# Optimization experiments

Hardware: AMD Instinct MI355X
Metric: run time of the kernel (lower is better)

The kernel has to match this reference:

```python
import jax, jax.numpy as jnp
import numpy as np

E = 8           # ensemble size
D_IN = 512      # input_dim (state+action)
H = 1024        # hidden size, arch=[1024, 1024]
D_OUT = 1       # output_dim (Q value)
LN_EPS = 1e-5


def setup_inputs() -> dict:
    key = jax.random.key(0)
    ks = jax.random.split(key, 8)
    s1 = 1.0 / np.sqrt(D_IN)
    s2 = 1.0 / np.sqrt(H)
    return {
        "x": jax.random.normal(ks[0], (16384, D_IN), dtype=jnp.float32),
        # stacked per-ensemble parameters: leading axis E
        "W1": jax.random.uniform(ks[1], (E, D_IN, H), jnp.float32, -s1, s1),
        "b1": jax.random.uniform(ks[2], (E, H), jnp.float32, -s1, s1),
        "g1": jnp.ones((E, H), jnp.float32),
        "be1": jnp.zeros((E, H), jnp.float32),
        "W2": jax.random.uniform(ks[3], (E, H, H), jnp.float32, -s2, s2),
        "b2": jax.random.uniform(ks[4], (E, H), jnp.float32, -s2, s2),
        "g2": jnp.ones((E, H), jnp.float32),
        "be2": jnp.zeros((E, H), jnp.float32),
        "W3": jax.random.uniform(ks[5], (E, H, D_OUT), jnp.float32, -s2, s2),
        "b3": jax.random.uniform(ks[6], (E, D_OUT), jnp.float32, -s2, s2),
    }


def _layer_norm(h, g, b):
    # h: [E, B, H]; g, b: [E, H] -> broadcast over batch
    mu = jnp.mean(h, axis=-1, keepdims=True)
    var = jnp.mean(jnp.square(h - mu), axis=-1, keepdims=True)
    return (h - mu) * jax.lax.rsqrt(var + LN_EPS) * g[:, None, :] + b[:, None, :]


def reference(x, W1, b1, g1, be1, W2, b2, g2, be2, W3, b3):
    # Layer 1: all ensemble members as one batched GEMM on shared input
    h = jnp.einsum('bd,edh->ebh', x, W1) + b1[:, None, :]       # [E, B, H]
    h = jax.nn.relu(_layer_norm(h, g1, be1))
    # Layer 2
    h = jnp.einsum('ebd,edh->ebh', h, W2) + b2[:, None, :]      # [E, B, H]
    h = jax.nn.relu(_layer_norm(h, g2, be2))
    # Head (identity head activation)
    qs = jnp.einsum('ebd,edo->ebo', h, W3) + b3[:, None, :]      # [E, B, 1]
    q = jnp.min(qs, axis=0)                                      # [B, 1]
    return (q, qs)
```

## Files before the change

### kernel.cpp

```cpp
#include <hip/hip_runtime.h>
#include <hip/hip_bf16.h>
#include <stdint.h>

#define EN    8
#define DIN   512
#define HID   1024
#define BATCH 16384
#define LN_EPS 1e-5f

typedef __bf16   bf16x8 __attribute__((ext_vector_type(8)));
typedef float    f32x4  __attribute__((ext_vector_type(4)));
typedef uint16_t u16x8  __attribute__((ext_vector_type(8)));
typedef uint16_t u16x4  __attribute__((ext_vector_type(4)));
typedef float    fl4    __attribute__((ext_vector_type(4)));

__device__ __forceinline__ uint16_t f2bf(float f) {
  uint32_t x = __builtin_bit_cast(uint32_t, f);
  uint32_t r = (x + 0x7fffu + ((x >> 16) & 1u)) >> 16;
  return (uint16_t)r;
}
__device__ __forceinline__ float bf2f(uint16_t u) {
  return __builtin_bit_cast(float, (uint32_t)u << 16);
}

__device__ __forceinline__ void gload16(const uint16_t* g, char* lds_d) {
  __builtin_amdgcn_global_load_lds(
      (const __attribute__((address_space(1))) uint32_t*)g,
      (__attribute__((address_space(3))) uint32_t*)lds_d, 16, 0, 0);
}

__device__ __forceinline__ f32x4 MF(bf16x8 a, bf16x8 b, f32x4 c) {
  return __builtin_amdgcn_mfma_f32_16x16x32_bf16(a, b, c, 0, 0, 0);
}

#define SB0() __builtin_amdgcn_sched_barrier(0)

__global__ __launch_bounds__(256) void cvt_bf16(const float* __restrict__ src,
                                                uint16_t* __restrict__ dst, long n) {
  long i = ((long)blockIdx.x * 256 + threadIdx.x) * 4;
  if (i >= n) return;
  fl4 v = *(const fl4*)(src + i);
  u16x4 o;
  #pragma unroll
  for (int j = 0; j < 4; ++j) o[j] = f2bf(v[j]);
  *(u16x4*)(dst + i) = o;
}

__global__ __launch_bounds__(256) void transpose_cvt(const float* __restrict__ src,
                                                     uint16_t* __restrict__ dst,
                                                     int R, int C) {
  __shared__ float tile[32][33];
  const int e = blockIdx.z;
  const int c0 = blockIdx.x * 32;
  const int r0 = blockIdx.y * 32;
  const int tx = threadIdx.x & 31, ty = threadIdx.x >> 5;
  const float* s = src + (size_t)e * R * C;
  uint16_t*    d = dst + (size_t)e * R * C;
  #pragma unroll
  for (int i = 0; i < 32; i += 8)
    tile[ty + i][tx] = s[(size_t)(r0 + ty + i) * C + (c0 + tx)];
  __syncthreads();
  #pragma unroll
  for (int i = 0; i < 32; i += 8)
    d[(size_t)(c0 + ty + i) * R + (r0 + tx)] = f2bf(tile[tx][ty + i]);
}

__global__ __launch_bounds__(256, 1) void gemm4w(
    const uint16_t* __restrict__ A, size_t a_estride,
    const uint16_t* __restrict__ Bt,
    const float*    __restrict__ bias,
    uint16_t*       __restrict__ C,
    int M, int K) {
  __shared__ __attribute__((aligned(16))) char lds[131072];
  const int tid = threadIdx.x;
  const int bx  = blockIdx.x;
  const int e   = bx & 7;
  const int t   = bx >> 3;
  const int mt  = t >> 2;
  const int nt  = t & 3;
  const int NT  = K >> 6;

  const uint16_t* Ae = A + (size_t)e * a_estride + (size_t)(mt * 256) * K;
  const uint16_t* Be = Bt + ((size_t)e * HID + nt * 256) * K;

  const int l  = tid & 63, wid = tid >> 6;
  const int wr = wid >> 1, wc = wid & 1;
  const int fr = l & 15, kq = l >> 4, f7 = fr & 7;

  const int r8 = l >> 3;
  const int su = (l & 7) ^ r8;
  const uint16_t* pA = Ae + (size_t)(wid * 8 + r8) * K + su * 8;
  const uint16_t* pB = Be + (size_t)(wid * 8 + r8) * K + su * 8;
  char* const dst0 = lds + tid * 16;

  const int rdA0 = (wr * 128 + fr) * 128 + ((kq ^ f7) << 4);
  const int rdB0 = 32768 + (wc * 128 + fr) * 128 + ((kq ^ f7) << 4);

  f32x4 acc[8][8];
  #pragma unroll
  for (int i = 0; i < 8; ++i)
    #pragma unroll
    for (int j = 0; j < 8; ++j) acc[i][j] = (f32x4)0.0f;

  auto STAGE = [&](int kt) {
    char* db = dst0 + ((kt & 1) << 16);
    const uint16_t* sa = pA + kt * 64;
    const uint16_t* sb = pB + kt * 64;
    #pragma unroll
    for (int j = 0; j < 8; ++j) gload16(sa + (size_t)(j * 32) * K, db + j * 4096);
    #pragma unroll
    for (int j = 0; j < 8; ++j) gload16(sb + (size_t)(j * 32) * K, db + 32768 + j * 4096);
  };

  STAGE(0);
  asm volatile("s_waitcnt vmcnt(0)");
  SB0();
  __builtin_amdgcn_s_barrier();
  SB0();

  bf16x8 a0[8], b0[8], a1[8], b1[8];
  {
    const char* rb = lds;
    #pragma unroll
    for (int i = 0; i < 8; ++i) {
      a0[i] = *(const bf16x8*)(rb + rdA0 + i * 2048);
      b0[i] = *(const bf16x8*)(rb + rdB0 + i * 2048);
    }
  }

  for (int kt = 0; kt < NT; ++kt) {
    const char* rb = lds + ((kt & 1) << 16);
    const char* rq = lds + (((kt + 1) & 1) << 16);
    if (kt + 1 < NT) STAGE(kt + 1);
    #pragma unroll
    for (int mi = 0; mi < 8; ++mi) {
      a1[mi] = *(const bf16x8*)(rb + ((rdA0 + mi * 2048) ^ 64));
      b1[mi] = *(const bf16x8*)(rb + ((rdB0 + mi * 2048) ^ 64));
      __builtin_amdgcn_s_setprio(1);
      #pragma unroll
      for (int ni = 0; ni < 8; ++ni)
        acc[mi][ni] = MF(a0[mi], b0[ni], acc[mi][ni]);
      __builtin_amdgcn_s_setprio(0);
    }
    #pragma unroll
    for (int mi = 0; mi < 8; ++mi) {
      __builtin_amdgcn_s_setprio(1);
      #pragma unroll
      for (int ni = 0; ni < 8; ++ni)
        acc[mi][ni] = MF(a1[mi], b1[ni], acc[mi][ni]);
      __builtin_amdgcn_s_setprio(0);
    }
    if (kt + 1 < NT) {
      asm volatile("s_waitcnt vmcnt(0)");
      SB0();
      __builtin_amdgcn_s_barrier();
      SB0();
      #pragma unroll
      for (int i = 0; i < 8; ++i) {
        a0[i] = *(const bf16x8*)(rq + rdA0 + i * 2048);
        b0[i] = *(const bf16x8*)(rq + rdB0 + i * 2048);
      }
    }
  }

  const int col0 = nt * 256 + wc * 128 + fr;
  const int row0 = mt * 256 + wr * 128 + kq * 4;
  float bv[8];
  #pragma unroll
  for (int ni = 0; ni < 8; ++ni) bv[ni] = bias[(size_t)e * HID + col0 + ni * 16];
  #pragma unroll
  for (int mi = 0; mi < 8; ++mi) {
    #pragma unroll
    for (int i = 0; i < 4; ++i) {
      const int rg = row0 + mi * 16 + i;
      uint16_t* cp = C + ((size_t)e * M + rg) * HID + col0;
      #pragma unroll
      for (int ni = 0; ni < 8; ++ni)
        cp[ni * 16] = f2bf(acc[mi][ni][i] + bv[ni]);
    }
  }
}

__global__ __launch_bounds__(256) void ln_relu(uint16_t* __restrict__ h,
                                               const float* __restrict__ g,
                                               const float* __restrict__ be,
                                               int kshift) {
  const int wid = threadIdx.x >> 6, l = threadIdx.x & 63;
  const long row = (long)blockIdx.x * 4 + wid;
  const int e = (int)(row >> kshift);
  uint16_t* p = h + row * HID;

  u16x8 s0 = *(const u16x8*)(p + l * 8);
  u16x8 s1 = *(const u16x8*)(p + 512 + l * 8);
  float v[16];
  #pragma unroll
  for (int j = 0; j < 8; ++j) { v[j] = bf2f(s0[j]); v[8 + j] = bf2f(s1[j]); }

  float sum = 0.f, sq = 0.f;
  #pragma unroll
  for (int j = 0; j < 16; ++j) { sum += v[j]; sq += v[j] * v[j]; }
  #pragma unroll
  for (int m = 1; m < 64; m <<= 1) {
    sum += __shfl_xor(sum, m);
    sq  += __shfl_xor(sq, m);
  }
  const float mu  = sum * (1.0f / HID);
  const float var = sq * (1.0f / HID) - mu * mu;
  const float rs  = rsqrtf(var + LN_EPS);

  const float* gp = g  + (size_t)e * HID;
  const float* bp = be + (size_t)e * HID;
  u16x8 o0, o1;
  #pragma unroll
  for (int j = 0; j < 8; ++j) {
    const int c0 = l * 8 + j, c1 = 512 + l * 8 + j;
    float x0 = (v[j]     - mu) * rs * gp[c0] + bp[c0];
    float x1 = (v[8 + j] - mu) * rs * gp[c1] + bp[c1];
    o0[j] = f2bf(fmaxf(x0, 0.f));
    o1[j] = f2bf(fmaxf(x1, 0.f));
  }
  *(u16x8*)(p + l * 8) = o0;
  *(u16x8*)(p + 512 + l * 8) = o1;
}

__global__ __launch_bounds__(256) void ln_head(const uint16_t* __restrict__ h,
                                               const float* __restrict__ g,
                                               const float* __restrict__ be,
                                               const float* __restrict__ W3,
                                               const float* __restrict__ b3,
                                               float* __restrict__ out,
                                               int b0, int CB) {
  __shared__ float qsh[EN];
  const int wv = threadIdx.x >> 6, l = threadIdx.x & 63;
  const long b = blockIdx.x;
  #pragma unroll
  for (int ee = 0; ee < 2; ++ee) {
    const int e = wv + ee * 4;
    const uint16_t* p = h + ((size_t)e * CB + b) * HID;
    u16x8 s0 = *(const u16x8*)(p + l * 8);
    u16x8 s1 = *(const u16x8*)(p + 512 + l * 8);
    float v[16];
    #pragma unroll
    for (int j = 0; j < 8; ++j) { v[j] = bf2f(s0[j]); v[8 + j] = bf2f(s1[j]); }
    float sum = 0.f, sq = 0.f;
    #pragma unroll
    for (int j = 0; j < 16; ++j) { sum += v[j]; sq += v[j] * v[j]; }
    #pragma unroll
    for (int m = 1; m < 64; m <<= 1) {
      sum += __shfl_xor(sum, m);
      sq  += __shfl_xor(sq, m);
    }
    const float mu  = sum * (1.0f / HID);
    const float var = sq * (1.0f / HID) - mu * mu;
    const float rs  = rsqrtf(var + LN_EPS);
    const float* gp = g  + (size_t)e * HID;
    const float* bp = be + (size_t)e * HID;
    const float* w  = W3 + (size_t)e * HID;
    float dot = 0.f;
    #pragma unroll
    for (int j = 0; j < 8; ++j) {
      const int c0 = l * 8 + j, c1 = 512 + l * 8 + j;
      float x0 = fmaxf((v[j]     - mu) * rs * gp[c0] + bp[c0], 0.f);
      float x1 = fmaxf((v[8 + j] - mu) * rs * gp[c1] + bp[c1], 0.f);
      dot += x0 * w[c0] + x1 * w[c1];
    }
    #pragma unroll
    for (int m = 1; m < 64; m <<= 1) dot += __shfl_xor(dot, m);
    if (l == 0) {
      const float qe = dot + b3[e];
      qsh[e] = qe;
      out[BATCH + (size_t)e * BATCH + b0 + b] = qe;
    }
  }
  __syncthreads();
  if (threadIdx.x == 0) {
    float m = qsh[0];
    #pragma unroll
    for (int i = 1; i < EN; ++i) m = fminf(m, qsh[i]);
    out[b0 + b] = m;
  }
}

extern "C" void kernel_launch(void* const* d_in, const int* in_sizes, int n_in,
                              void* d_out, int out_size, void* d_ws, size_t ws_size,
                              hipStream_t stream) {
  const float* x   = (const float*)d_in[0];
  const float* W1  = (const float*)d_in[1];
  const float* b1  = (const float*)d_in[2];
  const float* g1  = (const float*)d_in[3];
  const float* be1 = (const float*)d_in[4];
  const float* W2  = (const float*)d_in[5];
  const float* b2  = (const float*)d_in[6];
  const float* g2  = (const float*)d_in[7];
  const float* be2 = (const float*)d_in[8];
  const float* W3  = (const float*)d_in[9];
  const float* b3  = (const float*)d_in[10];
  float* out = (float*)d_out;

  char* ws = (char*)d_ws;
  uint16_t* xb  = (uint16_t*)ws; ws += (size_t)BATCH * DIN * 2;
  uint16_t* w1t = (uint16_t*)ws; ws += (size_t)EN * DIN * HID * 2;
  uint16_t* w2t = (uint16_t*)ws; ws += (size_t)EN * HID * HID * 2;
  size_t fixed = (size_t)(ws - (char*)d_ws);

  size_t avail = (ws_size > fixed) ? (ws_size - fixed) : 0;
  const size_t per_row = 2ULL * EN * HID * 2ULL;
  int CB = BATCH;
  while (CB > 256 && (size_t)CB * per_row > avail) CB >>= 1;
  const int nchunks = BATCH / CB;
  const int kshift = __builtin_ctz(CB);

  uint16_t* h1 = (uint16_t*)ws; ws += (size_t)EN * CB * HID * 2;
  uint16_t* h2 = (uint16_t*)ws;

  cvt_bf16<<<(BATCH * DIN / 4 + 255) / 256, 256, 0, stream>>>(x, xb, (long)BATCH * DIN);
  transpose_cvt<<<dim3(HID / 32, DIN / 32, EN), 256, 0, stream>>>(W1, w1t, DIN, HID);
  transpose_cvt<<<dim3(HID / 32, HID / 32, EN), 256, 0, stream>>>(W2, w2t, HID, HID);

  const int gblocks = (CB / 256) * (HID / 256) * EN;

  for (int c = 0; c < nchunks; ++c) {
    const int b0 = c * CB;
    gemm4w<<<gblocks, 256, 0, stream>>>(xb + (size_t)b0 * DIN, (size_t)0,
                                        w1t, b1, h1, CB, DIN);
    ln_relu<<<(EN * CB) / 4, 256, 0, stream>>>(h1, g1, be1, kshift);
    gemm4w<<<gblocks, 256, 0, stream>>>(h1, (size_t)CB * HID,
                                        w2t, b2, h2, CB, HID);
    ln_head<<<CB, 256, 0, stream>>>(h2, g2, be2, W3, b3, out, b0, CB);
  }
}
```

Before: 659.8 us.

## Fuse layer-1 LayerNorm stats into GEMM1 epilogue and apply LN+ReLU in GEMM2 prologue

The GEMM1 epilogue now computes per-row partial sum and sum-of-squares over its 256-column tile and writes them to a partial buffer. A small reduce kernel turns the partials into mean and rstd. GEMM2 then applies normalization, affine and ReLU to the A tile as it loads it into LDS. This removes the separate ln_relu pass, which read and wrote h1 once more. The cost is that GEMM2's A path is now register loads plus VALU work instead of direct global-to-LDS loads, the setprio hints are dropped, and LN is applied redundantly by each of the four column-tile blocks.

```diff
diff --git a/kernel.cpp b/kernel.cpp
--- a/kernel.cpp
+++ b/kernel.cpp
@@ -65,8 +65,171 @@
     d[(size_t)(c0 + ty + i) * R + (r0 + tx)] = f2bf(tile[tx][ty + i]);
 }
 
-__global__ __launch_bounds__(256, 1) void gemm4w(
-    const uint16_t* __restrict__ A, size_t a_estride,
+__global__ __launch_bounds__(256, 1) void gemm4w_s1(
+    const uint16_t* __restrict__ A,
+    const uint16_t* __restrict__ Bt,
+    const float*    __restrict__ bias,
+    uint16_t*       __restrict__ C,
+    float2*         __restrict__ Spart,
+    int M, int K) {
+  __shared__ __attribute__((aligned(16))) char lds[131072];
+  const int tid = threadIdx.x;
+  const int bx  = blockIdx.x;
+  const int e   = bx & 7;
+  const int t   = bx >> 3;
+  const int mt  = t >> 2;
+  const int nt  = t & 3;
+  const int NT  = K >> 6;
+
+  const uint16_t* Ae = A + (size_t)(mt * 256) * K;
+  const uint16_t* Be = Bt + ((size_t)e * HID + nt * 256) * K;
+
+  const int l  = tid & 63, wid = tid >> 6;
+  const int wr = wid >> 1, wc = wid & 1;
+  const int fr = l & 15, kq = l >> 4, f7 = fr & 7;
+
+  const int r8 = l >> 3;
+  const int su = (l & 7) ^ r8;
+  const uint16_t* pA = Ae + (size_t)(wid * 8 + r8) * K + su * 8;
+  const uint16_t* pB = Be + (size_t)(wid * 8 + r8) * K + su * 8;
+  char* const dst0 = lds + tid * 16;
+
+  const int rdA0 = (wr * 128 + fr) * 128 + ((kq ^ f7) << 4);
+  const int rdB0 = 32768 + (wc * 128 + fr) * 128 + ((kq ^ f7) << 4);
+
+  f32x4 acc[8][8];
+  #pragma unroll
+  for (int i = 0; i < 8; ++i)
+    #pragma unroll
+    for (int j = 0; j < 8; ++j) acc[i][j] = (f32x4)0.0f;
+
+  auto STAGE = [&](int kt) {
+    char* db = dst0 + ((kt & 1) << 16);
+    const uint16_t* sa = pA + kt * 64;
+    const uint16_t* sb = pB + kt * 64;
+    #pragma unroll
+    for (int j = 0; j < 8; ++j) gload16(sa + (size_t)(j * 32) * K, db + j * 4096);
+    #pragma unroll
+    for (int j = 0; j < 8; ++j) gload16(sb + (size_t)(j * 32) * K, db + 32768 + j * 4096);
+  };
+
+  STAGE(0);
+  asm volatile("s_waitcnt vmcnt(0)");
+  SB0();
+  __builtin_amdgcn_s_barrier();
+  SB0();
+
+  bf16x8 a0[8], b0[8], a1[8], b1[8];
+  {
+    const char* rb = lds;
+    #pragma unroll
+    for (int i = 0; i < 8; ++i) {
+      a0[i] = *(const bf16x8*)(rb + rdA0 + i * 2048);
+      b0[i] = *(const bf16x8*)(rb + rdB0 + i * 2048);
+    }
+  }
+
+  for (int kt = 0; kt < NT; ++kt) {
+    const char* rb = lds + ((kt & 1) << 16);
+    const char* rq = lds + (((kt + 1) & 1) << 16);
+    if (kt + 1 < NT) STAGE(kt + 1);
+    #pragma unroll
+    for (int mi = 0; mi < 8; ++mi) {
+      a1[mi] = *(const bf16x8*)(rb + ((rdA0 + mi * 2048) ^ 64));
+      b1[mi] = *(const bf16x8*)(rb + ((rdB0 + mi * 2048) ^ 64));
+      __builtin_amdgcn_s_setprio(1);
+      #pragma unroll
+      for (int ni = 0; ni < 8; ++ni)
+        acc[mi][ni] = MF(a0[mi], b0[ni], acc[mi][ni]);
+      __builtin_amdgcn_s_setprio(0);
+    }
+    #pragma unroll
+    for (int mi = 0; mi < 8; ++mi) {
+      __builtin_amdgcn_s_setprio(1);
+      #pragma unroll
+      for (int ni = 0; ni < 8; ++ni)
+        acc[mi][ni] = MF(a1[mi], b1[ni], acc[mi][ni]);
+      __builtin_amdgcn_s_setprio(0);
+    }
+    if (kt + 1 < NT) {
+      asm volatile("s_waitcnt vmcnt(0)");
+      SB0();
+      __builtin_amdgcn_s_barrier();
+      SB0();
+      #pragma unroll
+      for (int i = 0; i < 8; ++i) {
+        a0[i] = *(const bf16x8*)(rq + rdA0 + i * 2048);
+        b0[i] = *(const bf16x8*)(rq + rdB0 + i * 2048);
+      }
+    }
+  }
+
+  const int col0 = nt * 256 + wc * 128 + fr;
+  const int row0 = mt * 256 + wr * 128 + kq * 4;
+  #pragma unroll
+  for (int ni = 0; ni < 8; ++ni) {
+    const float bv = bias[(size_t)e * HID + col0 + ni * 16];
+    #pragma unroll
+    for (int mi = 0; mi < 8; ++mi)
+      #pragma unroll
+      for (int i = 0; i < 4; ++i) acc[mi][ni][i] += bv;
+  }
+  #pragma unroll
+  for (int mi = 0; mi < 8; ++mi) {
+    #pragma unroll
+    for (int i = 0; i < 4; ++i) {
+      const int rg = row0 + mi * 16 + i;
+      uint16_t* cp = C + ((size_t)e * M + rg) * HID + col0;
+      #pragma unroll
+      for (int ni = 0; ni < 8; ++ni)
+        cp[ni * 16] = f2bf(acc[mi][ni][i]);
+    }
+  }
+
+  __syncthreads();
+  float2* red = (float2*)lds;
+  #pragma unroll
+  for (int mi = 0; mi < 8; ++mi)
+    #pragma unroll
+    for (int i = 0; i < 4; ++i) {
+      float s = 0.f, q = 0.f;
+      #pragma unroll
+      for (int ni = 0; ni < 8; ++ni) { const float v = acc[mi][ni][i]; s += v; q += v * v; }
+      #pragma unroll
+      for (int m = 1; m < 16; m <<= 1) { s += __shfl_xor(s, m); q += __shfl_xor(q, m); }
+      if (fr == 0) red[(wr * 2 + wc) * 128 + mi * 16 + kq * 4 + i] = make_float2(s, q);
+    }
+  __syncthreads();
+  if (tid < 256) {
+    const int rl = tid, wrx = rl >> 7, rr = rl & 127;
+    const float2 p0 = red[(wrx * 2 + 0) * 128 + rr];
+    const float2 p1 = red[(wrx * 2 + 1) * 128 + rr];
+    Spart[((size_t)nt * EN + e) * M + mt * 256 + rl] =
+        make_float2(p0.x + p1.x, p0.y + p1.y);
+  }
+}
+
+__global__ __launch_bounds__(256) void stats_reduce(const float2* __restrict__ S,
+                                                    float2* __restrict__ st,
+                                                    long n) {
+  const long i = (long)blockIdx.x * 256 + threadIdx.x;
+  if (i >= n) return;
+  float s = 0.f, q = 0.f;
+  #pragma unroll
+  for (int p = 0; p < 4; ++p) {
+    const float2 v = S[(size_t)p * n + i];
+    s += v.x; q += v.y;
+  }
+  const float mu = s * (1.f / HID);
+  const float vr = q * (1.f / HID) - mu * mu;
+  st[i] = make_float2(mu, rsqrtf(vr + LN_EPS));
+}
+
+__global__ __launch_bounds__(256, 1) void gemm4w_s2(
+    const uint16_t* __restrict__ A,
+    const float2*   __restrict__ st,
+    const float*    __restrict__ g,
+    const float*    __restrict__ be,
     const uint16_t* __restrict__ Bt,
     const float*    __restrict__ bias,
     uint16_t*       __restrict__ C,
@@ -80,7 +243,7 @@
   const int nt  = t & 3;
   const int NT  = K >> 6;
 
-  const uint16_t* Ae = A + (size_t)e * a_estride + (size_t)(mt * 256) * K;
+  const uint16_t* Ae = A + (size_t)e * M * K + (size_t)(mt * 256) * K;
   const uint16_t* Be = Bt + ((size_t)e * HID + nt * 256) * K;
 
   const int l  = tid & 63, wid = tid >> 6;
@@ -89,9 +252,19 @@
 
   const int r8 = l >> 3;
   const int su = (l & 7) ^ r8;
-  const uint16_t* pA = Ae + (size_t)(wid * 8 + r8) * K + su * 8;
-  const uint16_t* pB = Be + (size_t)(wid * 8 + r8) * K + su * 8;
+  const int rbase = wid * 8 + r8;
+  const uint16_t* pA = Ae + (size_t)rbase * K + su * 8;
+  const uint16_t* pB = Be + (size_t)rbase * K + su * 8;
   char* const dst0 = lds + tid * 16;
+
+  float mu8[8], rs8[8];
+  {
+    const float2* sb = st + (size_t)e * M + mt * 256 + rbase;
+    #pragma unroll
+    for (int j = 0; j < 8; ++j) { const float2 v = sb[j * 32]; mu8[j] = v.x; rs8[j] = v.y; }
+  }
+  const float* gcol = g  + (size_t)e * HID + su * 8;
+  const float* ecol = be + (size_t)e * HID + su * 8;
 
   const int rdA0 = (wr * 128 + fr) * 128 + ((kq ^ f7) << 4);
   const int rdB0 = 32768 + (wc * 128 + fr) * 128 + ((kq ^ f7) << 4);
@@ -102,21 +275,41 @@
     #pragma unroll
     for (int j = 0; j < 8; ++j) acc[i][j] = (f32x4)0.0f;
 
-  auto STAGE = [&](int kt) {
+  auto STAGE_B = [&](int kt) {
     char* db = dst0 + ((kt & 1) << 16);
-    const uint16_t* sa = pA + kt * 64;
     const uint16_t* sb = pB + kt * 64;
-    #pragma unroll
-    for (int j = 0; j < 8; ++j) gload16(sa + (size_t)(j * 32) * K, db + j * 4096);
     #pragma unroll
     for (int j = 0; j < 8; ++j) gload16(sb + (size_t)(j * 32) * K, db + 32768 + j * 4096);
   };
-
-  STAGE(0);
-  asm volatile("s_waitcnt vmcnt(0)");
-  SB0();
-  __builtin_amdgcn_s_barrier();
-  SB0();
+  u16x8 aw[8];
+  auto LOAD_A = [&](int kt) {
+    const uint16_t* sa = pA + kt * 64;
+    #pragma unroll
+    for (int j = 0; j < 8; ++j) aw[j] = *(const u16x8*)(sa + (size_t)(j * 32) * K);
+  };
+  auto APPLY_WRITE = [&](int kt) {
+    char* db = dst0 + ((kt & 1) << 16);
+    float gk[8], bk[8];
+    const float* gp = gcol + kt * 64;
+    const float* ep = ecol + kt * 64;
+    *(fl4*)&gk[0] = *(const fl4*)gp;  *(fl4*)&gk[4] = *(const fl4*)(gp + 4);
+    *(fl4*)&bk[0] = *(const fl4*)ep;  *(fl4*)&bk[4] = *(const fl4*)(ep + 4);
+    #pragma unroll
+    for (int j = 0; j < 8; ++j) {
+      u16x8 o;
+      #pragma unroll
+      for (int x = 0; x < 8; ++x) {
+        const float v = (bf2f(aw[j][x]) - mu8[j]) * rs8[j] * gk[x] + bk[x];
+        o[x] = f2bf(fmaxf(v, 0.f));
+      }
+      *(u16x8*)(db + j * 4096) = o;
+    }
+  };
+
+  STAGE_B(0);
+  LOAD_A(0);
+  APPLY_WRITE(0);
+  __syncthreads();
 
   bf16x8 a0[8], b0[8], a1[8], b1[8];
   {
@@ -131,30 +324,23 @@
   for (int kt = 0; kt < NT; ++kt) {
     const char* rb = lds + ((kt & 1) << 16);
     const char* rq = lds + (((kt + 1) & 1) << 16);
-    if (kt + 1 < NT) STAGE(kt + 1);
+    if (kt + 1 < NT) { STAGE_B(kt + 1); LOAD_A(kt + 1); }
     #pragma unroll
     for (int mi = 0; mi < 8; ++mi) {
       a1[mi] = *(const bf16x8*)(rb + ((rdA0 + mi * 2048) ^ 64));
       b1[mi] = *(const bf16x8*)(rb + ((rdB0 + mi * 2048) ^ 64));
-      __builtin_amdgcn_s_setprio(1);
       #pragma unroll
       for (int ni = 0; ni < 8; ++ni)
         acc[mi][ni] = MF(a0[mi], b0[ni], acc[mi][ni]);
-      __builtin_amdgcn_s_setprio(0);
-    }
-    #pragma unroll
-    for (int mi = 0; mi < 8; ++mi) {
-      __builtin_amdgcn_s_setprio(1);
+    }
+    #pragma unroll
+    for (int mi = 0; mi < 8; ++mi)
       #pragma unroll
       for (int ni = 0; ni < 8; ++ni)
         acc[mi][ni] = MF(a1[mi], b1[ni], acc[mi][ni]);
-      __builtin_amdgcn_s_setprio(0);
-    }
     if (kt + 1 < NT) {
-      asm volatile("s_waitcnt vmcnt(0)");
-      SB0();
-      __builtin_amdgcn_s_barrier();
-      SB0();
+      APPLY_WRITE(kt + 1);
+      __syncthreads();
       #pragma unroll
       for (int i = 0; i < 8; ++i) {
         a0[i] = *(const bf16x8*)(rq + rdA0 + i * 2048);
@@ -179,48 +365,6 @@
         cp[ni * 16] = f2bf(acc[mi][ni][i] + bv[ni]);
     }
   }
-}
-
-__global__ __launch_bounds__(256) void ln_relu(uint16_t* __restrict__ h,
-                                               const float* __restrict__ g,
-                                               const float* __restrict__ be,
-                                               int kshift) {
-  const int wid = threadIdx.x >> 6, l = threadIdx.x & 63;
-  const long row = (long)blockIdx.x * 4 + wid;
-  const int e = (int)(row >> kshift);
-  uint16_t* p = h + row * HID;
-
-  u16x8 s0 = *(const u16x8*)(p + l * 8);
-  u16x8 s1 = *(const u16x8*)(p + 512 + l * 8);
-  float v[16];
-  #pragma unroll
-  for (int j = 0; j < 8; ++j) { v[j] = bf2f(s0[j]); v[8 + j] = bf2f(s1[j]); }
-
-  float sum = 0.f, sq = 0.f;
-  #pragma unroll
-  for (int j = 0; j < 16; ++j) { sum += v[j]; sq += v[j] * v[j]; }
-  #pragma unroll
-  for (int m = 1; m < 64; m <<= 1) {
-    sum += __shfl_xor(sum, m);
-    sq  += __shfl_xor(sq, m);
-  }
-  const float mu  = sum * (1.0f / HID);
-  const float var = sq * (1.0f / HID) - mu * mu;
-  const float rs  = rsqrtf(var + LN_EPS);
-
-  const float* gp = g  + (size_t)e * HID;
-  const float* bp = be + (size_t)e * HID;
-  u16x8 o0, o1;
-  #pragma unroll
-  for (int j = 0; j < 8; ++j) {
-    const int c0 = l * 8 + j, c1 = 512 + l * 8 + j;
-    float x0 = (v[j]     - mu) * rs * gp[c0] + bp[c0];
-    float x1 = (v[8 + j] - mu) * rs * gp[c1] + bp[c1];
-    o0[j] = f2bf(fmaxf(x0, 0.f));
-    o1[j] = f2bf(fmaxf(x1, 0.f));
-  }
-  *(u16x8*)(p + l * 8) = o0;
-  *(u16x8*)(p + 512 + l * 8) = o1;
 }
 
 __global__ __launch_bounds__(256) void ln_head(const uint16_t* __restrict__ h,
@@ -304,28 +448,32 @@
   size_t fixed = (size_t)(ws - (char*)d_ws);
 
   size_t avail = (ws_size > fixed) ? (ws_size - fixed) : 0;
-  const size_t per_row = 2ULL * EN * HID * 2ULL;
+  const size_t per_row = 2ULL * EN * HID * 2ULL
+                       + 4ULL * EN * 8ULL
+                       + (size_t)EN * 8ULL;
   int CB = BATCH;
   while (CB > 256 && (size_t)CB * per_row > avail) CB >>= 1;
   const int nchunks = BATCH / CB;
-  const int kshift = __builtin_ctz(CB);
-
-  uint16_t* h1 = (uint16_t*)ws; ws += (size_t)EN * CB * HID * 2;
-  uint16_t* h2 = (uint16_t*)ws;
+
+  uint16_t* h1   = (uint16_t*)ws; ws += (size_t)EN * CB * HID * 2;
+  uint16_t* h2   = (uint16_t*)ws; ws += (size_t)EN * CB * HID * 2;
+  float2*   Sp   = (float2*)ws;   ws += 4ULL * EN * CB * 8;
+  float2*   stat = (float2*)ws;
 
   cvt_bf16<<<(BATCH * DIN / 4 + 255) / 256, 256, 0, stream>>>(x, xb, (long)BATCH * DIN);
   transpose_cvt<<<dim3(HID / 32, DIN / 32, EN), 256, 0, stream>>>(W1, w1t, DIN, HID);
   transpose_cvt<<<dim3(HID / 32, HID / 32, EN), 256, 0, stream>>>(W2, w2t, HID, HID);
 
   const int gblocks = (CB / 256) * (HID / 256) * EN;
+  const long nst = (long)EN * CB;
 
   for (int c = 0; c < nchunks; ++c) {
     const int b0 = c * CB;
-    gemm4w<<<gblocks, 256, 0, stream>>>(xb + (size_t)b0 * DIN, (size_t)0,
-                                        w1t, b1, h1, CB, DIN);
-    ln_relu<<<(EN * CB) / 4, 256, 0, stream>>>(h1, g1, be1, kshift);
-    gemm4w<<<gblocks, 256, 0, stream>>>(h1, (size_t)CB * HID,
-                                        w2t, b2, h2, CB, HID);
+    gemm4w_s1<<<gblocks, 256, 0, stream>>>(xb + (size_t)b0 * DIN, w1t, b1, h1,
+                                           Sp, CB, DIN);
+    stats_reduce<<<(int)((nst + 255) / 256), 256, 0, stream>>>(Sp, stat, nst);
+    gemm4w_s2<<<gblocks, 256, 0, stream>>>(h1, stat, g1, be1, w2t, b2, h2,
+                                           CB, HID);
     ln_head<<<CB, 256, 0, stream>>>(h2, g2, be2, W3, b3, out, b0, CB);
   }
 }
```

Result: slower. 810.0 us (+22.8%).

## Add 256x128-tile triple-buffered GEMM kernel for layer-2 with two blocks per CU

Applied to the files above, without the earlier changes.

Adds a new GEMM kernel for the second layer that uses a 256x128 output tile, a three-slot LDS ring with prefetch two k-steps ahead, and launch bounds requesting two blocks per CU. The previous layer-2 call used the 256x256 tile kernel. A smaller per-thread accumulator and two resident blocks are meant to raise occupancy and hide global-load latency better. The cost is lower arithmetic reuse per loaded byte and more blocks to schedule.

```diff
diff --git a/kernel.cpp b/kernel.cpp
--- a/kernel.cpp
+++ b/kernel.cpp
@@ -177,6 +177,102 @@
       #pragma unroll
       for (int ni = 0; ni < 8; ++ni)
         cp[ni * 16] = f2bf(acc[mi][ni][i] + bv[ni]);
+    }
+  }
+}
+
+__global__ __launch_bounds__(256, 2) void gemm_t2(
+    const uint16_t* __restrict__ A, size_t a_estride,
+    const uint16_t* __restrict__ Bt,
+    const float*    __restrict__ bias,
+    uint16_t*       __restrict__ C,
+    int M, int K) {
+  __shared__ __attribute__((aligned(16))) char lds[73728];
+  const int tid = threadIdx.x;
+  const int bx  = blockIdx.x;
+  const int e   = bx & 7;
+  const int t   = bx >> 3;
+  const int mt  = t >> 3;
+  const int nt  = t & 7;
+  const int NT  = K >> 5;
+
+  const uint16_t* Ae = A + (size_t)e * a_estride + (size_t)(mt * 256) * K;
+  const uint16_t* Be = Bt + ((size_t)e * HID + nt * 128) * K;
+
+  const int l  = tid & 63, wid = tid >> 6;
+  const int wr = wid >> 1, wc = wid & 1;
+  const int fr = l & 15, kq = l >> 4;
+
+  const int pl = (tid >> 3) & 7;
+  const int su = (tid & 7) ^ pl;
+  const int r0 = 2 * (tid >> 3) + (su >> 2);
+  const int j8 = (su & 3) * 8;
+  const uint16_t* pA = Ae + (size_t)r0 * K + j8;
+  const uint16_t* pB = Be + (size_t)r0 * K + j8;
+  char* const ldst = lds + tid * 16;
+
+  const int un   = (((fr & 1) << 2) | kq) ^ (fr >> 1);
+  const int aoff = (wr * 64 + (fr >> 1)) * 128 + un * 16;
+  const int boff = 16384 + (wc * 32 + (fr >> 1)) * 128 + un * 16;
+
+  f32x4 acc[8][4];
+  #pragma unroll
+  for (int i = 0; i < 8; ++i)
+    #pragma unroll
+    for (int j = 0; j < 4; ++j) acc[i][j] = (f32x4)0.0f;
+
+  auto STAGE = [&](int kt, int slot) {
+    char* db = ldst + slot * 24576;
+    const uint16_t* sa = pA + kt * 32;
+    const uint16_t* sb = pB + kt * 32;
+    #pragma unroll
+    for (int c = 0; c < 4; ++c) gload16(sa + (size_t)(c * 64) * K, db + c * 4096);
+    #pragma unroll
+    for (int c = 0; c < 2; ++c) gload16(sb + (size_t)(c * 64) * K, db + 16384 + c * 4096);
+  };
+
+  STAGE(0, 0);
+  STAGE(1, 1);
+  asm volatile("s_waitcnt vmcnt(6)");
+  __builtin_amdgcn_s_barrier();
+
+  int scur = 0;
+  for (int kt = 0; kt < NT; ++kt) {
+    if (kt + 2 < NT) {
+      int s2 = scur + 2; if (s2 >= 3) s2 -= 3;
+      STAGE(kt + 2, s2);
+    }
+    const char* rb = lds + scur * 24576;
+    bf16x8 af[8], bv[4];
+    #pragma unroll
+    for (int mi = 0; mi < 8; ++mi) af[mi] = *(const bf16x8*)(rb + aoff + mi * 1024);
+    #pragma unroll
+    for (int ni = 0; ni < 4; ++ni) bv[ni] = *(const bf16x8*)(rb + boff + ni * 1024);
+    #pragma unroll
+    for (int mi = 0; mi < 8; ++mi)
+      #pragma unroll
+      for (int ni = 0; ni < 4; ++ni)
+        acc[mi][ni] = MF(af[mi], bv[ni], acc[mi][ni]);
+    if (kt + 2 < NT)      asm volatile("s_waitcnt vmcnt(6)");
+    else if (kt + 1 < NT) asm volatile("s_waitcnt vmcnt(0)");
+    if (kt + 1 < NT) __builtin_amdgcn_s_barrier();
+    scur = (scur + 1 == 3) ? 0 : scur + 1;
+  }
+
+  const int col0 = nt * 128 + wc * 64 + fr;
+  const int row0 = mt * 256 + wr * 128 + kq * 4;
+  float bvv[4];
+  #pragma unroll
+  for (int ni = 0; ni < 4; ++ni) bvv[ni] = bias[(size_t)e * HID + col0 + ni * 16];
+  #pragma unroll
+  for (int mi = 0; mi < 8; ++mi) {
+    #pragma unroll
+    for (int i = 0; i < 4; ++i) {
+      const int rg = row0 + mi * 16 + i;
+      uint16_t* cp = C + ((size_t)e * M + rg) * HID + col0;
+      #pragma unroll
+      for (int ni = 0; ni < 4; ++ni)
+        cp[ni * 16] = f2bf(acc[mi][ni][i] + bvv[ni]);
     }
   }
 }
@@ -317,15 +413,16 @@
   transpose_cvt<<<dim3(HID / 32, DIN / 32, EN), 256, 0, stream>>>(W1, w1t, DIN, HID);
   transpose_cvt<<<dim3(HID / 32, HID / 32, EN), 256, 0, stream>>>(W2, w2t, HID, HID);
 
-  const int gblocks = (CB / 256) * (HID / 256) * EN;
+  const int g1blocks = (CB / 256) * (HID / 256) * EN;
+  const int g2blocks = (CB / 256) * (HID / 128) * EN;
 
   for (int c = 0; c < nchunks; ++c) {
     const int b0 = c * CB;
-    gemm4w<<<gblocks, 256, 0, stream>>>(xb + (size_t)b0 * DIN, (size_t)0,
-                                        w1t, b1, h1, CB, DIN);
+    gemm4w<<<g1blocks, 256, 0, stream>>>(xb + (size_t)b0 * DIN, (size_t)0,
+                                         w1t, b1, h1, CB, DIN);
     ln_relu<<<(EN * CB) / 4, 256, 0, stream>>>(h1, g1, be1, kshift);
-    gemm4w<<<gblocks, 256, 0, stream>>>(h1, (size_t)CB * HID,
-                                        w2t, b2, h2, CB, HID);
+    gemm_t2<<<g2blocks, 256, 0, stream>>>(h1, (size_t)CB * HID,
+                                          w2t, b2, h2, CB, HID);
     ln_head<<<CB, 256, 0, stream>>>(h2, g2, be2, W3, b3, out, b0, CB);
   }
 }
```

Result: no change. 671.0 us (+1.7%).
